# Kernel tuning notes

Hardware: AMD Instinct MI355X
Metric: run time of the kernel (lower is better)

The kernel has to match this reference:

```python
import jax, jax.numpy as jnp
import numpy as np

BINS = 256
MIN_V = -0.25
MAX_V = 1.25
XSIGMA = 1.0 / float(np.sqrt(2.0 * np.pi))
DELTA = (MAX_V - MIN_V) / BINS
SIGMA = DELTA * XSIGMA
# constant prefactor applied once to the joint kernel: delta / (sqrt(2*pi)*sigma)
COEF = float(DELTA / (np.sqrt(2.0 * np.pi) * SIGMA))

B, N = 8, 32768


def setup_inputs() -> dict:
    key = jax.random.key(0)
    k1, k2, k3 = jax.random.split(key, 3)
    x1 = jax.random.uniform(k1, (B, N), dtype=jnp.float32)
    x2 = jax.random.uniform(k2, (B, N), dtype=jnp.float32)
    mask = jax.random.uniform(k3, (B, N), dtype=jnp.float32)
    return {"x1": x1, "x2": x2, "mask": mask}


def reference(x1, x2, mask):
    # bin centers: (bins,)
    centers = MIN_V + DELTA * (jnp.arange(BINS, dtype=x1.dtype) + 0.5)
    inv_s = 1.0 / SIGMA
    # Separable factorization of exp(-0.5*((x1-ci)^2+(x2-cj)^2)/sigma^2):
    # g1: (b, bins, N), g2: (b, bins, N) with mask folded into g2.
    d1 = (x1[:, None, :] - centers[None, :, None]) * inv_s
    d2 = (x2[:, None, :] - centers[None, :, None]) * inv_s
    g1 = jnp.exp(-0.5 * d1 * d1)
    g2 = jnp.exp(-0.5 * d2 * d2) * mask[:, None, :]
    # contract over N via batched matmul -> (b, bins, bins)
    hist = jnp.einsum("bin,bjn->bij", g1, g2)
    return COEF * hist
```

## Files before the change

kernel.cpp:

```cpp
#include <hip/hip_runtime.h>


#define BINS   256
#define NPTS   32768
#define BATCH  8
#define TROWS  16
#define NTILE  (BINS / TROWS)
#define CHUNK  4
#define PPC    (NPTS / CHUNK)
#define WORDS  64
#define TILE64 (2 * TROWS * WORDS)

static constexpr float kInvDelta = 256.0f / 1.5f;
static constexpr float kUAdd     = 0.25f * (256.0f / 1.5f) - 0.5f;
static constexpr float kPi       = 3.14159265358979323846f;
static constexpr float kFix      = 1024.0f;
static constexpr float kInvFix   = 1.0f / 1024.0f;

__global__ __launch_bounds__(512) void gh_part(
    const float* __restrict__ x1, const float* __restrict__ x2,
    const float* __restrict__ mask, unsigned long long* __restrict__ ws)
{
    __shared__ unsigned long long tile[TILE64];
    const int tid = threadIdx.x;
    const int t   = blockIdx.x;
    const int b   = blockIdx.y;
    const int z   = blockIdx.z;
    const int r0  = t * TROWS;

#pragma unroll
    for (int i = tid; i < TILE64; i += 512) tile[i] = 0ULL;
    __syncthreads();

    const float4* X1 = (const float4*)(x1   + b * NPTS + z * PPC);
    const float4* X2 = (const float4*)(x2   + b * NPTS + z * PPC);
    const float4* M  = (const float4*)(mask + b * NPTS + z * PPC);

#pragma unroll 2
    for (int it = 0; it < PPC / 2048; ++it) {
        const int n4 = it * 512 + tid;
        const float4 a4 = X1[n4];
        const float4 b4 = X2[n4];
        const float4 m4 = M[n4];

        const float pv1[4] = {a4.x, a4.y, a4.z, a4.w};
        const float pv2[4] = {b4.x, b4.y, b4.z, b4.w};
        const float pm[4]  = {m4.x, m4.y, m4.z, m4.w};

#pragma unroll
        for (int k = 0; k < 4; ++k) {
            const float u1 = fmaf(pv1[k], kInvDelta, kUAdd);
            const float u2 = fmaf(pv2[k], kInvDelta, kUAdd);
            const float fi = rintf(u1);
            const int   i0 = (int)fi;
            const float t1 = u1 - fi;

            int e = (((int)rintf(u2)) - 1) & ~1;
            e = min(250, max(0, e));
            const int  ph   = (e >> 1) & 1;
            const int  word = e >> 2;
            const float t2  = u2 - (float)e;

            float w1a[3];
#pragma unroll
            for (int a = 0; a < 3; ++a) {
                const float d = t1 - (float)(a - 1);
                w1a[a] = __expf(-kPi * d * d);
            }
            float W2[4];
#pragma unroll
            for (int c = 0; c < 4; ++c) {
                const float d = t2 - (float)c;
                W2[c] = __expf(-kPi * d * d) * (pm[k] * kFix);
            }

            const int rbase = i0 - 1 - r0;
            const int pbase = ph * (TROWS * WORDS) + word;
#pragma unroll
            for (int a = 0; a < 3; ++a) {
                const int r = rbase + a;
                if ((unsigned)r < TROWS) {
                    const float wa = w1a[a];
                    const unsigned f0 = (unsigned)fmaf(wa, W2[0], 0.5f);
                    const unsigned f1 = (unsigned)fmaf(wa, W2[1], 0.5f);
                    const unsigned f2 = (unsigned)fmaf(wa, W2[2], 0.5f);
                    const unsigned f3 = (unsigned)fmaf(wa, W2[3], 0.5f);
                    const unsigned long long w =
                        (unsigned long long)(f0 | (f1 << 16)) |
                        ((unsigned long long)(f2 | (f3 << 16)) << 32);
                    atomicAdd(&tile[pbase + r * WORDS], w);
                }
            }
        }
    }
    __syncthreads();

    unsigned long long* W = ws + (size_t)((b * NTILE + t) * CHUNK + z) * TILE64;
#pragma unroll
    for (int i = tid; i < TILE64; i += 512) W[i] = tile[i];
}

__global__ __launch_bounds__(1024) void gh_reduce(
    const unsigned long long* __restrict__ ws, float* __restrict__ out)
{
    const int g     = blockIdx.x * 1024 + threadIdx.x;
    const int cell0 = g * 2;
    const int b     = cell0 >> 16;
    const int rem   = cell0 & 65535;
    const int r     = rem >> 8;
    const int c0    = rem & 255;
    const int t     = r >> 4;
    const int rr    = r & 15;

    const unsigned long long* W = ws + (size_t)((b * NTILE + t) * CHUNK) * TILE64;
    unsigned a0 = 0, a1 = 0;
#pragma unroll
    for (int z = 0; z < CHUNK; ++z) {
        const unsigned long long* Z = W + z * TILE64;
        const unsigned long long we = Z[rr * WORDS + (c0 >> 2)];
        a0 += (unsigned)(we >> (16 * (c0 & 3)))       & 0xFFFFu;
        a1 += (unsigned)(we >> (16 * ((c0 + 1) & 3))) & 0xFFFFu;
        if (c0 >= 2) {
            const unsigned long long wo =
                Z[TROWS * WORDS + rr * WORDS + ((c0 - 2) >> 2)];
            a0 += (unsigned)(wo >> (16 * ((c0 - 2) & 3))) & 0xFFFFu;
            a1 += (unsigned)(wo >> (16 * ((c0 - 1) & 3))) & 0xFFFFu;
        }
    }
    float2 f;
    f.x = (float)a0 * kInvFix;
    f.y = (float)a1 * kInvFix;
    *(float2*)(out + (size_t)cell0) = f;
}

extern "C" void kernel_launch(void* const* d_in, const int* in_sizes, int n_in,
                              void* d_out, int out_size, void* d_ws, size_t ws_size,
                              hipStream_t stream) {
    const float* x1   = (const float*)d_in[0];
    const float* x2   = (const float*)d_in[1];
    const float* mask = (const float*)d_in[2];
    float*       out  = (float*)d_out;
    unsigned long long* ws = (unsigned long long*)d_ws;

    gh_part<<<dim3(NTILE, BATCH, CHUNK), 512, 0, stream>>>(x1, x2, mask, ws);
    gh_reduce<<<dim3(BATCH * BINS * BINS / 2048), 1024, 0, stream>>>(ws, out);
}
```

Before: 75.38 us.

## Replace LDS row-tiled histogram with direct global 64-bit atomics

Drops the per-block LDS tiles, where each block re-read every point of its chunk for only 16 bin rows. Each thread now reads its points once and atomically adds packed fixed-point weights straight into a per-batch global histogram, which a separate kernel zeroes first. This removes the 16x redundant input reads and the multi-chunk reduction. In exchange, about 3 global 64-bit atomics per point go to a small, heavily contended region, and a third kernel launch is added. It also clamps i0 to [1,254], which changes edge handling.

```diff
diff --git a/kernel.cpp b/kernel.cpp
--- a/kernel.cpp
+++ b/kernel.cpp
@@ -4,12 +4,8 @@
 #define BINS   256
 #define NPTS   32768
 #define BATCH  8
-#define TROWS  16
-#define NTILE  (BINS / TROWS)
-#define CHUNK  4
-#define PPC    (NPTS / CHUNK)
 #define WORDS  64
-#define TILE64 (2 * TROWS * WORDS)
+#define WSU64  (BATCH * 2 * BINS * WORDS)
 
 static constexpr float kInvDelta = 256.0f / 1.5f;
 static constexpr float kUAdd     = 0.25f * (256.0f / 1.5f) - 0.5f;
@@ -17,90 +13,75 @@
 static constexpr float kFix      = 1024.0f;
 static constexpr float kInvFix   = 1.0f / 1024.0f;
 
-__global__ __launch_bounds__(512) void gh_part(
+__global__ __launch_bounds__(1024) void gh_zero(unsigned long long* __restrict__ ws)
+{
+    ws[blockIdx.x * 1024 + threadIdx.x] = 0ULL;
+}
+
+__global__ __launch_bounds__(256) void gh_scatter(
     const float* __restrict__ x1, const float* __restrict__ x2,
     const float* __restrict__ mask, unsigned long long* __restrict__ ws)
 {
-    __shared__ unsigned long long tile[TILE64];
-    const int tid = threadIdx.x;
-    const int t   = blockIdx.x;
-    const int b   = blockIdx.y;
-    const int z   = blockIdx.z;
-    const int r0  = t * TROWS;
+    const int g  = blockIdx.x * 256 + threadIdx.x;
+    const int b  = g >> 13;
+    const int n4 = g & 8191;
+
+    const float4 a4 = ((const float4*)(x1   + b * NPTS))[n4];
+    const float4 b4 = ((const float4*)(x2   + b * NPTS))[n4];
+    const float4 m4 = ((const float4*)(mask + b * NPTS))[n4];
+
+    const float pv1[4] = {a4.x, a4.y, a4.z, a4.w};
+    const float pv2[4] = {b4.x, b4.y, b4.z, b4.w};
+    const float pm[4]  = {m4.x, m4.y, m4.z, m4.w};
+
+    unsigned long long* WB = ws + (size_t)b * (2 * BINS * WORDS);
 
 #pragma unroll
-    for (int i = tid; i < TILE64; i += 512) tile[i] = 0ULL;
-    __syncthreads();
+    for (int k = 0; k < 4; ++k) {
+        const float u1 = fmaf(pv1[k], kInvDelta, kUAdd);
+        const float u2 = fmaf(pv2[k], kInvDelta, kUAdd);
+        const float fi = rintf(u1);
+        int i0 = (int)fi;
+        i0 = min(254, max(1, i0));
+        const float t1 = u1 - fi;
 
-    const float4* X1 = (const float4*)(x1   + b * NPTS + z * PPC);
-    const float4* X2 = (const float4*)(x2   + b * NPTS + z * PPC);
-    const float4* M  = (const float4*)(mask + b * NPTS + z * PPC);
+        int e = (((int)rintf(u2)) - 1) & ~1;
+        e = min(250, max(0, e));
+        const int  ph   = (e >> 1) & 1;
+        const int  word = e >> 2;
+        const float t2  = u2 - (float)e;
 
-#pragma unroll 2
-    for (int it = 0; it < PPC / 2048; ++it) {
-        const int n4 = it * 512 + tid;
-        const float4 a4 = X1[n4];
-        const float4 b4 = X2[n4];
-        const float4 m4 = M[n4];
+        float w1a[3];
+#pragma unroll
+        for (int a = 0; a < 3; ++a) {
+            const float d = t1 - (float)(a - 1);
+            w1a[a] = __expf(-kPi * d * d);
+        }
+        float W2[4];
+#pragma unroll
+        for (int c = 0; c < 4; ++c) {
+            const float d = t2 - (float)c;
+            W2[c] = __expf(-kPi * d * d) * (pm[k] * kFix);
+        }
 
-        const float pv1[4] = {a4.x, a4.y, a4.z, a4.w};
-        const float pv2[4] = {b4.x, b4.y, b4.z, b4.w};
-        const float pm[4]  = {m4.x, m4.y, m4.z, m4.w};
-
+        unsigned long long* P = WB + (size_t)ph * (BINS * WORDS) + word;
 #pragma unroll
-        for (int k = 0; k < 4; ++k) {
-            const float u1 = fmaf(pv1[k], kInvDelta, kUAdd);
-            const float u2 = fmaf(pv2[k], kInvDelta, kUAdd);
-            const float fi = rintf(u1);
-            const int   i0 = (int)fi;
-            const float t1 = u1 - fi;
-
-            int e = (((int)rintf(u2)) - 1) & ~1;
-            e = min(250, max(0, e));
-            const int  ph   = (e >> 1) & 1;
-            const int  word = e >> 2;
-            const float t2  = u2 - (float)e;
-
-            float w1a[3];
-#pragma unroll
-            for (int a = 0; a < 3; ++a) {
-                const float d = t1 - (float)(a - 1);
-                w1a[a] = __expf(-kPi * d * d);
-            }
-            float W2[4];
-#pragma unroll
-            for (int c = 0; c < 4; ++c) {
-                const float d = t2 - (float)c;
-                W2[c] = __expf(-kPi * d * d) * (pm[k] * kFix);
-            }
-
-            const int rbase = i0 - 1 - r0;
-            const int pbase = ph * (TROWS * WORDS) + word;
-#pragma unroll
-            for (int a = 0; a < 3; ++a) {
-                const int r = rbase + a;
-                if ((unsigned)r < TROWS) {
-                    const float wa = w1a[a];
-                    const unsigned f0 = (unsigned)fmaf(wa, W2[0], 0.5f);
-                    const unsigned f1 = (unsigned)fmaf(wa, W2[1], 0.5f);
-                    const unsigned f2 = (unsigned)fmaf(wa, W2[2], 0.5f);
-                    const unsigned f3 = (unsigned)fmaf(wa, W2[3], 0.5f);
-                    const unsigned long long w =
-                        (unsigned long long)(f0 | (f1 << 16)) |
-                        ((unsigned long long)(f2 | (f3 << 16)) << 32);
-                    atomicAdd(&tile[pbase + r * WORDS], w);
-                }
-            }
+        for (int a = 0; a < 3; ++a) {
+            const int r = i0 - 1 + a;
+            const float wa = w1a[a];
+            const unsigned f0 = (unsigned)fmaf(wa, W2[0], 0.5f);
+            const unsigned f1 = (unsigned)fmaf(wa, W2[1], 0.5f);
+            const unsigned f2 = (unsigned)fmaf(wa, W2[2], 0.5f);
+            const unsigned f3 = (unsigned)fmaf(wa, W2[3], 0.5f);
+            const unsigned long long w =
+                (unsigned long long)(f0 | (f1 << 16)) |
+                ((unsigned long long)(f2 | (f3 << 16)) << 32);
+            atomicAdd(&P[(size_t)r * WORDS], w);
         }
     }
-    __syncthreads();
-
-    unsigned long long* W = ws + (size_t)((b * NTILE + t) * CHUNK + z) * TILE64;
-#pragma unroll
-    for (int i = tid; i < TILE64; i += 512) W[i] = tile[i];
 }
 
-__global__ __launch_bounds__(1024) void gh_reduce(
+__global__ __launch_bounds__(1024) void gh_unpack(
     const unsigned long long* __restrict__ ws, float* __restrict__ out)
 {
     const int g     = blockIdx.x * 1024 + threadIdx.x;
@@ -109,23 +90,16 @@
     const int rem   = cell0 & 65535;
     const int r     = rem >> 8;
     const int c0    = rem & 255;
-    const int t     = r >> 4;
-    const int rr    = r & 15;
 
-    const unsigned long long* W = ws + (size_t)((b * NTILE + t) * CHUNK) * TILE64;
-    unsigned a0 = 0, a1 = 0;
-#pragma unroll
-    for (int z = 0; z < CHUNK; ++z) {
-        const unsigned long long* Z = W + z * TILE64;
-        const unsigned long long we = Z[rr * WORDS + (c0 >> 2)];
-        a0 += (unsigned)(we >> (16 * (c0 & 3)))       & 0xFFFFu;
-        a1 += (unsigned)(we >> (16 * ((c0 + 1) & 3))) & 0xFFFFu;
-        if (c0 >= 2) {
-            const unsigned long long wo =
-                Z[TROWS * WORDS + rr * WORDS + ((c0 - 2) >> 2)];
-            a0 += (unsigned)(wo >> (16 * ((c0 - 2) & 3))) & 0xFFFFu;
-            a1 += (unsigned)(wo >> (16 * ((c0 - 1) & 3))) & 0xFFFFu;
-        }
+    const unsigned long long* WB = ws + (size_t)b * (2 * BINS * WORDS);
+    const unsigned long long we = WB[(size_t)r * WORDS + (c0 >> 2)];
+    unsigned a0 = (unsigned)(we >> (16 * (c0 & 3)))       & 0xFFFFu;
+    unsigned a1 = (unsigned)(we >> (16 * ((c0 + 1) & 3))) & 0xFFFFu;
+    if (c0 >= 2) {
+        const unsigned long long wo =
+            WB[(size_t)(BINS * WORDS) + r * WORDS + ((c0 - 2) >> 2)];
+        a0 += (unsigned)(wo >> (16 * ((c0 - 2) & 3))) & 0xFFFFu;
+        a1 += (unsigned)(wo >> (16 * ((c0 - 1) & 3))) & 0xFFFFu;
     }
     float2 f;
     f.x = (float)a0 * kInvFix;
@@ -142,6 +116,7 @@
     float*       out  = (float*)d_out;
     unsigned long long* ws = (unsigned long long*)d_ws;
 
-    gh_part<<<dim3(NTILE, BATCH, CHUNK), 512, 0, stream>>>(x1, x2, mask, ws);
-    gh_reduce<<<dim3(BATCH * BINS * BINS / 2048), 1024, 0, stream>>>(ws, out);
+    gh_zero   <<<dim3(WSU64 / 1024), 1024, 0, stream>>>(ws);
+    gh_scatter<<<dim3(BATCH * NPTS / 4 / 256), 256, 0, stream>>>(x1, x2, mask, ws);
+    gh_unpack <<<dim3(BATCH * BINS * BINS / 2048), 1024, 0, stream>>>(ws, out);
 }
```

Result: slower. 95.66 us (+26.9%).

## Fuse partial histogram and reduction into one cooperative kernel with fewer exps

Applied to the files above, without the earlier changes.

Merges the two launches into a single cooperative kernel: each block writes its partial tile, does a grid-wide sync, then reduces a slice of rows directly to the output. Row tiles grow from 16 to 32, so there are half as many tiles per batch and each point is re-read fewer times. The seven Gaussian exps per point are replaced by four exps plus reciprocals, using a recurrence for neighbouring bins with closed-form constants. The trade-off is a grid barrier that requires all 256 blocks to be resident, a larger LDS tile, and slightly different rounding in the weights.

```diff
diff --git a/kernel.cpp b/kernel.cpp
--- a/kernel.cpp
+++ b/kernel.cpp
@@ -1,31 +1,41 @@
 #include <hip/hip_runtime.h>
+#include <hip/hip_cooperative_groups.h>
+
+namespace cg = cooperative_groups;
 
 
 #define BINS   256
 #define NPTS   32768
 #define BATCH  8
-#define TROWS  16
+#define TROWS  32
 #define NTILE  (BINS / TROWS)
 #define CHUNK  4
 #define PPC    (NPTS / CHUNK)
 #define WORDS  64
 #define TILE64 (2 * TROWS * WORDS)
+#define NBLK   (BATCH * NTILE * CHUNK)
 
 static constexpr float kInvDelta = 256.0f / 1.5f;
 static constexpr float kUAdd     = 0.25f * (256.0f / 1.5f) - 0.5f;
 static constexpr float kPi       = 3.14159265358979323846f;
+static constexpr float kTwoPi    = 6.28318530717958647692f;
+static constexpr float kEmPi     = 0.043213918263772250f;
+static constexpr float kC1       = 0.4559381277659962f;
+static constexpr float kC2       = 8.514366756432101e-4f;
 static constexpr float kFix      = 1024.0f;
 static constexpr float kInvFix   = 1.0f / 1024.0f;
 
-__global__ __launch_bounds__(512) void gh_part(
+__global__ __launch_bounds__(512, 2) void gh_all(
     const float* __restrict__ x1, const float* __restrict__ x2,
-    const float* __restrict__ mask, unsigned long long* __restrict__ ws)
+    const float* __restrict__ mask, unsigned long long* __restrict__ ws,
+    float* __restrict__ out)
 {
     __shared__ unsigned long long tile[TILE64];
     const int tid = threadIdx.x;
-    const int t   = blockIdx.x;
-    const int b   = blockIdx.y;
-    const int z   = blockIdx.z;
+    const int blk = blockIdx.x;
+    const int b   = blk >> 5;
+    const int t   = (blk >> 2) & 7;
+    const int z   = blk & 3;
     const int r0  = t * TROWS;
 
 #pragma unroll
@@ -36,7 +46,7 @@
     const float4* X2 = (const float4*)(x2   + b * NPTS + z * PPC);
     const float4* M  = (const float4*)(mask + b * NPTS + z * PPC);
 
-#pragma unroll 2
+#pragma unroll
     for (int it = 0; it < PPC / 2048; ++it) {
         const int n4 = it * 512 + tid;
         const float4 a4 = X1[n4];
@@ -52,39 +62,45 @@
             const float u1 = fmaf(pv1[k], kInvDelta, kUAdd);
             const float u2 = fmaf(pv2[k], kInvDelta, kUAdd);
             const float fi = rintf(u1);
-            const int   i0 = (int)fi;
+            int i0 = (int)fi;
+            i0 = min(254, max(1, i0));
             const float t1 = u1 - fi;
 
             int e = (((int)rintf(u2)) - 1) & ~1;
             e = min(250, max(0, e));
             const int  ph   = (e >> 1) & 1;
             const int  word = e >> 2;
-            const float t2  = u2 - (float)e;
+            const float s   = (u2 - (float)e) - 1.5f;
 
-            float w1a[3];
-#pragma unroll
-            for (int a = 0; a < 3; ++a) {
-                const float d = t1 - (float)(a - 1);
-                w1a[a] = __expf(-kPi * d * d);
-            }
-            float W2[4];
-#pragma unroll
-            for (int c = 0; c < 4; ++c) {
-                const float d = t2 - (float)c;
-                W2[c] = __expf(-kPi * d * d) * (pm[k] * kFix);
-            }
+            const float w0  = __expf(-kPi * t1 * t1);
+            const float E   = __expf(-kTwoPi * t1);
+            const float iE  = __builtin_amdgcn_rcpf(E);
+            const float w0K = w0 * kEmPi;
+            const float wr0 = w0K * E;
+            const float wr2 = w0K * iE;
+
+            const float P   = __expf(-kPi * s * s);
+            const float Q   = __expf(-kPi * s);
+            const float iQ  = __builtin_amdgcn_rcpf(Q);
+            const float Q3  = Q * Q * Q;
+            const float iQ3 = iQ * iQ * iQ;
+            const float pmF = pm[k] * kFix;
+            const float PC1 = P * (kC1 * pmF);
+            const float PC2 = P * (kC2 * pmF);
+            const float W0 = PC2 * Q3, W1 = PC1 * Q, W2v = PC1 * iQ, W3 = PC2 * iQ3;
 
             const int rbase = i0 - 1 - r0;
             const int pbase = ph * (TROWS * WORDS) + word;
+            const float wra[3] = {wr0, w0, wr2};
 #pragma unroll
             for (int a = 0; a < 3; ++a) {
                 const int r = rbase + a;
                 if ((unsigned)r < TROWS) {
-                    const float wa = w1a[a];
-                    const unsigned f0 = (unsigned)fmaf(wa, W2[0], 0.5f);
-                    const unsigned f1 = (unsigned)fmaf(wa, W2[1], 0.5f);
-                    const unsigned f2 = (unsigned)fmaf(wa, W2[2], 0.5f);
-                    const unsigned f3 = (unsigned)fmaf(wa, W2[3], 0.5f);
+                    const float wa = wra[a];
+                    const unsigned f0 = (unsigned)fmaf(wa, W0, 0.5f);
+                    const unsigned f1 = (unsigned)fmaf(wa, W1, 0.5f);
+                    const unsigned f2 = (unsigned)fmaf(wa, W2v, 0.5f);
+                    const unsigned f3 = (unsigned)fmaf(wa, W3, 0.5f);
                     const unsigned long long w =
                         (unsigned long long)(f0 | (f1 << 16)) |
                         ((unsigned long long)(f2 | (f3 << 16)) << 32);
@@ -95,42 +111,42 @@
     }
     __syncthreads();
 
-    unsigned long long* W = ws + (size_t)((b * NTILE + t) * CHUNK + z) * TILE64;
+    {
+        unsigned long long* W = ws + (size_t)blk * TILE64;
 #pragma unroll
-    for (int i = tid; i < TILE64; i += 512) W[i] = tile[i];
-}
+        for (int i = tid; i < TILE64; i += 512) W[i] = tile[i];
+    }
+    __threadfence();
+    cg::this_grid().sync();
+    __threadfence();
 
-__global__ __launch_bounds__(1024) void gh_reduce(
-    const unsigned long long* __restrict__ ws, float* __restrict__ out)
-{
-    const int g     = blockIdx.x * 1024 + threadIdx.x;
-    const int cell0 = g * 2;
-    const int b     = cell0 >> 16;
-    const int rem   = cell0 & 65535;
-    const int r     = rem >> 8;
-    const int c0    = rem & 255;
-    const int t     = r >> 4;
-    const int rr    = r & 15;
-
-    const unsigned long long* W = ws + (size_t)((b * NTILE + t) * CHUNK) * TILE64;
-    unsigned a0 = 0, a1 = 0;
+    const int r_l = tid >> 7;
+    const int c0  = (tid & 127) * 2;
 #pragma unroll
-    for (int z = 0; z < CHUNK; ++z) {
-        const unsigned long long* Z = W + z * TILE64;
-        const unsigned long long we = Z[rr * WORDS + (c0 >> 2)];
-        a0 += (unsigned)(we >> (16 * (c0 & 3)))       & 0xFFFFu;
-        a1 += (unsigned)(we >> (16 * ((c0 + 1) & 3))) & 0xFFFFu;
-        if (c0 >= 2) {
-            const unsigned long long wo =
-                Z[TROWS * WORDS + rr * WORDS + ((c0 - 2) >> 2)];
-            a0 += (unsigned)(wo >> (16 * ((c0 - 2) & 3))) & 0xFFFFu;
-            a1 += (unsigned)(wo >> (16 * ((c0 - 1) & 3))) & 0xFFFFu;
+    for (int ii = 0; ii < 2; ++ii) {
+        const int rt = z * 8 + r_l + ii * 4;
+        unsigned a0 = 0, a1 = 0;
+#pragma unroll
+        for (int zz = 0; zz < CHUNK; ++zz) {
+            const unsigned long long* Zp =
+                ws + (size_t)(((b * NTILE + t) * CHUNK + zz)) * TILE64;
+            const unsigned long long we = Zp[rt * WORDS + (c0 >> 2)];
+            const int sh = 16 * (c0 & 3);
+            a0 += (unsigned)(we >> sh)        & 0xFFFFu;
+            a1 += (unsigned)(we >> (sh + 16)) & 0xFFFFu;
+            if (c0 >= 2) {
+                const unsigned long long wo =
+                    Zp[TROWS * WORDS + rt * WORDS + ((c0 - 2) >> 2)];
+                const int sho = 16 * ((c0 - 2) & 3);
+                a0 += (unsigned)(wo >> sho)        & 0xFFFFu;
+                a1 += (unsigned)(wo >> (sho + 16)) & 0xFFFFu;
+            }
         }
+        float2 f;
+        f.x = (float)a0 * kInvFix;
+        f.y = (float)a1 * kInvFix;
+        *(float2*)(out + ((size_t)b * BINS + r0 + rt) * BINS + c0) = f;
     }
-    float2 f;
-    f.x = (float)a0 * kInvFix;
-    f.y = (float)a1 * kInvFix;
-    *(float2*)(out + (size_t)cell0) = f;
 }
 
 extern "C" void kernel_launch(void* const* d_in, const int* in_sizes, int n_in,
@@ -142,6 +158,7 @@
     float*       out  = (float*)d_out;
     unsigned long long* ws = (unsigned long long*)d_ws;
 
-    gh_part<<<dim3(NTILE, BATCH, CHUNK), 512, 0, stream>>>(x1, x2, mask, ws);
-    gh_reduce<<<dim3(BATCH * BINS * BINS / 2048), 1024, 0, stream>>>(ws, out);
+    void* args[] = {(void*)&x1, (void*)&x2, (void*)&mask, (void*)&ws, (void*)&out};
+    (void)hipLaunchCooperativeKernel((const void*)gh_all, dim3(NBLK), dim3(512),
+                                     args, 0, stream);
 }
```

New measurement: 183.1 us. 143% more time.
